# Performance work log

Hardware: AMD Instinct MI355X
Metric: run time of the kernel (lower is better)

Reference implementation:

```python
import jax, jax.numpy as jnp
import numpy as np

# ---------------- geometry constants (from init_kwargs) ----------------
N_PROJ = 96          # cone-beam projections (batch of 2D BP, views of 3D BP)
A2D    = 96          # 2D parallel angles (= detector rows of cone sinogram)
DET2D  = 192         # 2D detector bins   (= detector cols of cone sinogram)
DS2D   = 1.0         # 2D detector spacing
H = 128
W = 128              # intermediate CB_projection image (geom_2d volume)
Zd = 128
Yd = 128
Xd = 128             # reconstruction volume (geometry.volume_shape)
DSO = 500.0          # source-isocenter distance
DSD = 1000.0         # source-detector distance
DU = 3.5
DV = 3.5             # 3D detector spacing (detector grid == H x W image grid)


def _grad_lastdim(x):
    # torch.gradient(x, dim=-1) with unit spacing: central diffs, one-sided edges
    left = x[..., 1:2] - x[..., 0:1]
    mid = (x[..., 2:] - x[..., :-2]) * 0.5
    right = x[..., -1:] - x[..., -2:-1]
    return jnp.concatenate([left, mid, right], axis=-1)


def _image_grid(h, w):
    ys = jnp.arange(h, dtype=jnp.float32) - (h - 1) / 2.0
    xs = jnp.arange(w, dtype=jnp.float32) - (w - 1) / 2.0
    yg, xg = jnp.meshgrid(ys, xs, indexing='ij')  # [h, w]
    return yg, xg


def _weights_3d():
    # Defrise-Clack intermediate-function weighting: cosine of ray angle,
    # w(x,y) = D / sqrt(D^2 + x^2 + y^2) on the intermediate image grid.
    yg, xg = _image_grid(H, W)
    return DSD / jnp.sqrt(DSD * DSD + xg * xg + yg * yg)


def _bp2d(sino):
    # Pixel-driven 2D parallel backprojection, batched over N.
    # sino: [N, A2D, DET2D] -> [N, H, W]
    yg, xg = _image_grid(H, W)
    th = jnp.arange(A2D, dtype=jnp.float32) * (np.pi / A2D)
    s = jnp.cos(th)[:, None, None] * xg + jnp.sin(th)[:, None, None] * yg  # [A,H,W]
    pos = s / DS2D + (DET2D - 1) / 2.0
    i0 = jnp.floor(pos).astype(jnp.int32)
    f = pos - i0
    i1 = i0 + 1
    w0 = jnp.where((i0 >= 0) & (i0 < DET2D), 1.0 - f, 0.0)
    w1 = jnp.where((i1 >= 0) & (i1 < DET2D), f, 0.0)
    i0c = jnp.clip(i0, 0, DET2D - 1)
    i1c = jnp.clip(i1, 0, DET2D - 1)
    aa = jnp.arange(A2D)[:, None, None]  # [A,1,1]
    g0 = sino[:, aa, i0c]  # [N, A, H, W]
    g1 = sino[:, aa, i1c]
    return (g0 * w0 + g1 * w1).sum(axis=1)  # [N, H, W]


def _bp3d(projs):
    # Voxel-driven circular cone-beam backprojection with FDK distance weight.
    # projs: [N_PROJ, H, W] (V=H rows, U=W cols) -> volume [Zd, Yd, Xd]
    zs = jnp.arange(Zd, dtype=jnp.float32) - (Zd - 1) / 2.0
    ys = jnp.arange(Yd, dtype=jnp.float32) - (Yd - 1) / 2.0
    xs = jnp.arange(Xd, dtype=jnp.float32) - (Xd - 1) / 2.0
    zz, yy, xx = jnp.meshgrid(zs, ys, xs, indexing='ij')  # [Z,Y,X]
    betas = jnp.arange(N_PROJ, dtype=jnp.float32) * (2.0 * np.pi / N_PROJ)

    def body(acc, inp):
        beta, proj = inp
        cb, sb = jnp.cos(beta), jnp.sin(beta)
        t = xx * cb + yy * sb          # along central ray
        s = -xx * sb + yy * cb         # transaxial offset
        r = DSO + t                    # source-to-voxel-plane distance
        pu = (DSD * s / r) / DU + (W - 1) / 2.0
        pv = (DSD * zz / r) / DV + (H - 1) / 2.0
        iu0 = jnp.floor(pu).astype(jnp.int32); fu = pu - iu0; iu1 = iu0 + 1
        iv0 = jnp.floor(pv).astype(jnp.int32); fv = pv - iv0; iv1 = iv0 + 1
        mu0 = (iu0 >= 0) & (iu0 < W); mu1 = (iu1 >= 0) & (iu1 < W)
        mv0 = (iv0 >= 0) & (iv0 < H); mv1 = (iv1 >= 0) & (iv1 < H)
        iu0c = jnp.clip(iu0, 0, W - 1); iu1c = jnp.clip(iu1, 0, W - 1)
        iv0c = jnp.clip(iv0, 0, H - 1); iv1c = jnp.clip(iv1, 0, H - 1)
        w00 = jnp.where(mv0 & mu0, (1 - fv) * (1 - fu), 0.0)
        w01 = jnp.where(mv0 & mu1, (1 - fv) * fu, 0.0)
        w10 = jnp.where(mv1 & mu0, fv * (1 - fu), 0.0)
        w11 = jnp.where(mv1 & mu1, fv * fu, 0.0)
        val = (proj[iv0c, iu0c] * w00 + proj[iv0c, iu1c] * w01 +
               proj[iv1c, iu0c] * w10 + proj[iv1c, iu1c] * w11)
        acc = acc + val * (DSD / r) ** 2
        return acc, None

    acc, _ = jax.lax.scan(body, jnp.zeros((Zd, Yd, Xd), jnp.float32), (betas, projs))
    return acc


def setup_inputs() -> dict:
    key = jax.random.key(0)
    k1, k2 = jax.random.split(key)
    sinogram = jax.random.normal(k1, (1, 1, N_PROJ, A2D, DET2D), dtype=jnp.float32)
    weight = jax.random.uniform(k2, (1, N_PROJ, A2D, DET2D), dtype=jnp.float32)
    prelu_weight = jnp.full((1,), 0.25, dtype=jnp.float32)
    return {"sinogram": sinogram, "weight": weight, "prelu_weight": prelu_weight}


def reference(sinogram, weight, prelu_weight):
    ws = sinogram[0] * weight                 # [1, N, A, D]
    deriv = _grad_lastdim(ws)[0]              # [N, A, D]  (squeeze dim 0)
    cb = _bp2d(deriv)                         # [N, H, W]
    weighted_cb = cb * _weights_3d()          # [N, H, W]
    reco = _bp3d(weighted_cb)[None]           # [1, Z, Y, X]
    a = prelu_weight[0]
    return jnp.where(reco >= 0, reco, a * reco)  # PReLU (single parameter)
```

## Files before the change

### kernel.cpp

```cpp
#include <hip/hip_runtime.h>
#include <hip/hip_fp16.h>
#include <math.h>

#define NPROJ 96
#define NANG  96
#define DET   192
#define NPIX  16384
#define SLICE (NANG*DET)

#define WQROW0   16
#define WQROWS   96
#define WQSLICEB (WQROWS*128*16)

#define KPROJ 285.7142857142857f

__device__ __forceinline__ float frcp(float x) { return __builtin_amdgcn_rcpf(x); }

__device__ __forceinline__ float ffract(float x) {
#if __has_builtin(__builtin_amdgcn_fractf)
    return __builtin_amdgcn_fractf(x);
#else
    return x - floorf(x);
#endif
}

typedef __fp16 h2 __attribute__((ext_vector_type(2)));

__device__ __forceinline__ unsigned pack2(float a, float b) {
    h2 p = __builtin_amdgcn_cvt_pkrtz(a, b);
    return __builtin_bit_cast(unsigned, p);
}
__device__ __forceinline__ h2 as_h2(unsigned u) { return __builtin_bit_cast(h2, u); }

#if __has_builtin(__builtin_amdgcn_fdot2)
#define FDOT2(a, b, c) __builtin_amdgcn_fdot2((a), (b), (c), false)
#else
__device__ __forceinline__ float FDOT2(h2 a, h2 b, float c) {
    return c + (float)a[0] * (float)b[0] + (float)a[1] * (float)b[1];
}
#endif

__global__ __launch_bounds__(192) void k_deriv(const float* __restrict__ sino,
                                               const float* __restrict__ wgt,
                                               unsigned* __restrict__ derivp) {
    __shared__ float row[DET];
    const int r = blockIdx.x;
    const int d = threadIdx.x;
    const int base = r * DET + d;
    row[d] = sino[base] * wgt[base];
    __syncthreads();
    auto grad = [&](int i) -> float {
        i = (i > DET-1) ? DET-1 : i;
        if (i == 0)       return row[1] - row[0];
        if (i == DET-1)   return row[DET-1] - row[DET-2];
        return 0.5f * (row[i+1] - row[i-1]);
    };
    const float g0 = grad(d), g1 = grad(d+1);
    derivp[base] = pack2(g0, g1 - g0);
}

__global__ __launch_bounds__(256) void k_bp2d(const unsigned* __restrict__ derivp,
                                              unsigned* __restrict__ wq_dw,
                                              uint2* __restrict__ tbl) {
    __shared__ float sc[NANG], ss[NANG];
    __shared__ float buf[512];
    const int p   = blockIdx.x;
    const int tid = threadIdx.x;

    if (tid < NANG) {
        float s_, c_;
        sincosf((float)tid * (float)(3.14159265358979323846 / 96.0), &s_, &c_);
        sc[tid] = c_; ss[tid] = s_;
    }

    float sb2, cb2;
    sincosf((float)p * (float)(2.0 * 3.14159265358979323846 / 96.0), &sb2, &cb2);

    const int pixbase = blockIdx.y * 512;
    float acc[2], fx[2], fy[2];
    #pragma unroll
    for (int i = 0; i < 2; ++i) {
        const int pix = pixbase + i*256 + tid;
        fx[i] = (float)(pix & 127) - 63.5f;
        fy[i] = (float)(pix >> 7)  - 63.5f;
        acc[i] = 0.0f;
    }
    __syncthreads();

    const unsigned* rowp = derivp + p * SLICE;
    for (int a = 0; a < NANG; ++a, rowp += DET) {
        const float cb = sc[a], sb = ss[a];
        #pragma unroll
        for (int i = 0; i < 2; ++i) {
            const float pos = fmaf(cb, fx[i], fmaf(sb, fy[i], 95.5f));
            const int   i0  = (int)pos;
            const float f   = ffract(pos);
            acc[i] = FDOT2(as_h2(rowp[i0]), as_h2(pack2(1.0f, f)), acc[i]);
        }
    }

    #pragma unroll
    for (int i = 0; i < 2; ++i) {
        const float w = 1000.0f * rsqrtf(1000000.0f + fx[i]*fx[i] + fy[i]*fy[i]);
        buf[i*256 + tid] = acc[i] * w;
    }
    __syncthreads();

    unsigned* sq = wq_dw + p * (WQROWS * 128 * 4);
    uint2*    tp = tbl   + p * NPIX;
    #pragma unroll
    for (int i = 0; i < 2; ++i) {
        const int l   = i*256 + tid;
        const int pix = pixbase + l;
        const int u   = pix & 127;
        const int v   = pix >> 7;
        const float v0 = buf[l];
        const float v1 = (u < 127) ? buf[l + 1] : 0.0f;
        const unsigned pr = pack2(v0, v1 - v0);
        #pragma unroll
        for (int k = 0; k < 4; ++k) {
            const int vb = v - k;
            if (vb >= WQROW0 && vb < WQROW0 + WQROWS)
                sq[(((vb - WQROW0) << 7) + u) << 2 | k] = pr;
        }
        const float t3   = fmaf(fx[i], cb2,  fy[i] * sb2);
        const float sd3  = fmaf(fy[i], cb2, -fx[i] * sb2);
        const float invr = frcp(500.0f + t3);
        const float pu   = fmaf(KPROJ * sd3, invr, 63.5f);
        const int   iu0  = (int)pu;
        const float fu   = ffract(pu);
        float w2 = 1000.0f * invr; w2 *= w2;
        const float Kz   = KPROJ * invr;
        const unsigned kzi = (__builtin_bit_cast(unsigned, Kz) & ~127u) | (unsigned)iu0;
        uint2 e; e.x = pack2(w2, fu * w2); e.y = kzi;
        tp[pix] = e;
    }
}

struct QS {
    uint4    q0, q1;
    unsigned wuw;
    float    fvA0, fvB0, fvA1, fvB1;
    int      d0, d1;
};

__global__ __launch_bounds__(256, 8) void k_bp3d_t2(const unsigned char* __restrict__ wq,
                                                    const unsigned char* __restrict__ tbl8,
                                                    const float* __restrict__ prelu,
                                                    float* __restrict__ out) {
    const int tid = threadIdx.x;
    const int x   = tid & 127;
    const int y   = (blockIdx.x << 1) | (tid >> 7);
    const int z0  = blockIdx.y << 2;
    const int pix = (y << 7) + x;

    const float zlo = (float)z0 - 63.5f;

    float acc[4];
    #pragma unroll
    for (int j = 0; j < 4; ++j) acc[j] = 0.0f;

    const unsigned pixoff = ((unsigned)pix) << 3;

    auto TLOAD = [&](int b) -> uint2 {
        return *(const uint2*)(tbl8 + (pixoff + (unsigned)b * (NPIX * 8u)));
    };

    auto ISSUE = [&](QS& S, uint2 T, int b) {
        S.wuw = T.x;
        const int   iu0 = (int)(T.y & 127u);
        const float Kz  = __builtin_bit_cast(float, T.y & ~127u);
        const unsigned sbase = (unsigned)b * (unsigned)WQSLICEB
                             + (unsigned)(iu0 << 4) - (unsigned)(WQROW0 << 11);

        const float pvA0 = fmaf(Kz, zlo, 63.5f);
        const float pvB0 = pvA0 + Kz;
        const int   ivA0 = (int)pvA0;
        S.d0   = (int)pvB0 - ivA0;
        S.fvA0 = ffract(pvA0);
        S.fvB0 = ffract(pvB0);
        S.q0   = *(const uint4*)(wq + (sbase + ((unsigned)ivA0 << 11)));

        const float pvA1 = fmaf(Kz, zlo + 2.0f, 63.5f);
        const float pvB1 = pvA1 + Kz;
        const int   ivA1 = (int)pvA1;
        S.d1   = (int)pvB1 - ivA1;
        S.fvA1 = ffract(pvA1);
        S.fvB1 = ffract(pvB1);
        S.q1   = *(const uint4*)(wq + (sbase + ((unsigned)ivA1 << 11)));
    };

    auto MATH = [&](const QS& S) {
        const h2 wuw = as_h2(S.wuw);
        {
            const float tA = FDOT2(as_h2(S.q0.x), wuw, 0.0f);
            const float bA = FDOT2(as_h2(S.q0.y), wuw, 0.0f);
            acc[0] += fmaf(S.fvA0, bA - tA, tA);
            const unsigned tBv = S.d0 ? S.q0.y : S.q0.x;
            const unsigned bBv = S.d0 ? S.q0.z : S.q0.y;
            const float tB = FDOT2(as_h2(tBv), wuw, 0.0f);
            const float bB = FDOT2(as_h2(bBv), wuw, 0.0f);
            acc[1] += fmaf(S.fvB0, bB - tB, tB);
        }
        {
            const float tA = FDOT2(as_h2(S.q1.x), wuw, 0.0f);
            const float bA = FDOT2(as_h2(S.q1.y), wuw, 0.0f);
            acc[2] += fmaf(S.fvA1, bA - tA, tA);
            const unsigned tBv = S.d1 ? S.q1.y : S.q1.x;
            const unsigned bBv = S.d1 ? S.q1.z : S.q1.y;
            const float tB = FDOT2(as_h2(tBv), wuw, 0.0f);
            const float bB = FDOT2(as_h2(bBv), wuw, 0.0f);
            acc[3] += fmaf(S.fvB1, bB - tB, tB);
        }
    };

    QS qa, qb;
    uint2 Ta = TLOAD(0);
    uint2 Tb = TLOAD(1);
    ISSUE(qa, Ta, 0);
    for (int b = 0; b < 94; b += 2) {
        Ta = TLOAD(b + 2);
        ISSUE(qb, Tb, b + 1);
        MATH(qa);
        Tb = TLOAD(b + 3);
        ISSUE(qa, Ta, b + 2);
        MATH(qb);
    }
    ISSUE(qb, Tb, 95);
    MATH(qa);
    MATH(qb);

    const float a = prelu[0];
    #pragma unroll
    for (int j = 0; j < 4; ++j) {
        const float v = acc[j];
        out[((z0 + j) << 14) + (y << 7) + x] = (v >= 0.0f) ? v : a * v;
    }
}

extern "C" void kernel_launch(void* const* d_in, const int* in_sizes, int n_in,
                              void* d_out, int out_size, void* d_ws, size_t ws_size,
                              hipStream_t stream) {
    const float* sino  = (const float*)d_in[0];
    const float* wgt   = (const float*)d_in[1];
    const float* prelu = (const float*)d_in[2];
    float* out = (float*)d_out;

    unsigned char* wsb = (unsigned char*)d_ws;
    unsigned* wq_dw  = (unsigned*)wsb;
    uint2*    tbl    = (uint2*)(wsb + (size_t)NPROJ * WQSLICEB);
    unsigned* derivp = (unsigned*)(wsb + (size_t)NPROJ * WQSLICEB
                                       + (size_t)NPROJ * NPIX * 8);

    k_deriv  <<<dim3(NPROJ * NANG), dim3(192), 0, stream>>>(sino, wgt, derivp);
    k_bp2d   <<<dim3(NPROJ, 32),    dim3(256), 0, stream>>>(derivp, wq_dw, tbl);
    k_bp3d_t2<<<dim3(64, 32),       dim3(256), 0, stream>>>((const unsigned char*)wq_dw,
                                                            (const unsigned char*)tbl, prelu, out);
}
```

Measured before the change: 180.5 us.

## Batch derivative rows per block and share 2D BP geometry across four projections

The derivative kernel now processes 16 sinogram rows per 256-thread block instead of one 192-thread block per row, which cuts launch granularity. The 2D backprojection kernel gives each thread one pixel across four projections. The per-angle position, index and fraction are computed once and reused for four gathers, so address arithmetic is amortised and there are more independent loads in flight. The trade-off is fewer pixels per thread, higher register use and a different grid shape for the bp2d stage. The 3D backprojection, which likely dominates the runtime, is unchanged.

```diff
diff --git a/kernel.cpp b/kernel.cpp
--- a/kernel.cpp
+++ b/kernel.cpp
@@ -7,6 +7,7 @@
 #define DET   192
 #define NPIX  16384
 #define SLICE (NANG*DET)
+#define NROWS (NPROJ*NANG)
 
 #define WQROW0   16
 #define WQROWS   96
@@ -40,91 +41,111 @@
 }
 #endif
 
-__global__ __launch_bounds__(192) void k_deriv(const float* __restrict__ sino,
-                                               const float* __restrict__ wgt,
-                                               unsigned* __restrict__ derivp) {
-    __shared__ float row[DET];
-    const int r = blockIdx.x;
-    const int d = threadIdx.x;
-    const int base = r * DET + d;
-    row[d] = sino[base] * wgt[base];
+__global__ __launch_bounds__(256) void k_deriv16(const float* __restrict__ sino,
+                                                 const float* __restrict__ wgt,
+                                                 unsigned* __restrict__ derivp) {
+    __shared__ float sw[16 * DET];
+    const int tid   = threadIdx.x;
+    const int base0 = blockIdx.x * (16 * DET);
+
+    #pragma unroll
+    for (int k = 0; k < 12; ++k) {
+        const int i = k * 256 + tid;
+        sw[i] = sino[base0 + i] * wgt[base0 + i];
+    }
     __syncthreads();
-    auto grad = [&](int i) -> float {
-        i = (i > DET-1) ? DET-1 : i;
-        if (i == 0)       return row[1] - row[0];
-        if (i == DET-1)   return row[DET-1] - row[DET-2];
-        return 0.5f * (row[i+1] - row[i-1]);
-    };
-    const float g0 = grad(d), g1 = grad(d+1);
-    derivp[base] = pack2(g0, g1 - g0);
-}
-
-__global__ __launch_bounds__(256) void k_bp2d(const unsigned* __restrict__ derivp,
-                                              unsigned* __restrict__ wq_dw,
-                                              uint2* __restrict__ tbl) {
+
+    #pragma unroll
+    for (int k = 0; k < 12; ++k) {
+        const int i = k * 256 + tid;
+        const int r = i / DET;
+        const int d = i - r * DET;
+        const float* row = sw + r * DET;
+        auto grad = [&](int q) -> float {
+            if (q == 0)        return row[1] - row[0];
+            if (q >= DET - 1)  return row[DET-1] - row[DET-2];
+            return 0.5f * (row[q+1] - row[q-1]);
+        };
+        const float g0 = grad(d), g1 = grad(d + 1);
+        derivp[base0 + i] = pack2(g0, g1 - g0);
+    }
+}
+
+__global__ __launch_bounds__(256) void k_bp2d_p4(const unsigned* __restrict__ derivp,
+                                                 unsigned* __restrict__ wq_dw,
+                                                 uint2* __restrict__ tbl) {
     __shared__ float sc[NANG], ss[NANG];
-    __shared__ float buf[512];
-    const int p   = blockIdx.x;
+    __shared__ float sc3[4], ss3[4];
+    __shared__ float buf[4][257];
     const int tid = threadIdx.x;
+    const int p0  = blockIdx.y << 2;
+    const int pix = (blockIdx.x << 8) + tid;
+    const int u   = pix & 127;
+    const int v   = pix >> 7;
 
     if (tid < NANG) {
         float s_, c_;
         sincosf((float)tid * (float)(3.14159265358979323846 / 96.0), &s_, &c_);
         sc[tid] = c_; ss[tid] = s_;
     }
-
-    float sb2, cb2;
-    sincosf((float)p * (float)(2.0 * 3.14159265358979323846 / 96.0), &sb2, &cb2);
-
-    const int pixbase = blockIdx.y * 512;
-    float acc[2], fx[2], fy[2];
-    #pragma unroll
-    for (int i = 0; i < 2; ++i) {
-        const int pix = pixbase + i*256 + tid;
-        fx[i] = (float)(pix & 127) - 63.5f;
-        fy[i] = (float)(pix >> 7)  - 63.5f;
-        acc[i] = 0.0f;
-    }
+    if (tid < 4) {
+        float s_, c_;
+        sincosf((float)(p0 + tid) * (float)(2.0 * 3.14159265358979323846 / 96.0), &s_, &c_);
+        sc3[tid] = c_; ss3[tid] = s_;
+    }
+
+    const float fx = (float)u - 63.5f;
+    const float fy = (float)v - 63.5f;
+
+    float acc[4];
+    #pragma unroll
+    for (int j = 0; j < 4; ++j) acc[j] = 0.0f;
+
     __syncthreads();
 
-    const unsigned* rowp = derivp + p * SLICE;
-    for (int a = 0; a < NANG; ++a, rowp += DET) {
+    const unsigned* b0 = derivp + (p0 + 0) * SLICE;
+    const unsigned* b1 = derivp + (p0 + 1) * SLICE;
+    const unsigned* b2 = derivp + (p0 + 2) * SLICE;
+    const unsigned* b3 = derivp + (p0 + 3) * SLICE;
+
+    int aoff = 0;
+    #pragma unroll 2
+    for (int a = 0; a < NANG; ++a, aoff += DET) {
         const float cb = sc[a], sb = ss[a];
-        #pragma unroll
-        for (int i = 0; i < 2; ++i) {
-            const float pos = fmaf(cb, fx[i], fmaf(sb, fy[i], 95.5f));
-            const int   i0  = (int)pos;
-            const float f   = ffract(pos);
-            acc[i] = FDOT2(as_h2(rowp[i0]), as_h2(pack2(1.0f, f)), acc[i]);
-        }
-    }
-
-    #pragma unroll
-    for (int i = 0; i < 2; ++i) {
-        const float w = 1000.0f * rsqrtf(1000000.0f + fx[i]*fx[i] + fy[i]*fy[i]);
-        buf[i*256 + tid] = acc[i] * w;
+        const float pos = fmaf(cb, fx, fmaf(sb, fy, 95.5f));
+        const int   i0  = (int)pos;
+        const float f   = ffract(pos);
+        const h2    wv  = as_h2(pack2(1.0f, f));
+        const int   idx = aoff + i0;
+        acc[0] = FDOT2(as_h2(b0[idx]), wv, acc[0]);
+        acc[1] = FDOT2(as_h2(b1[idx]), wv, acc[1]);
+        acc[2] = FDOT2(as_h2(b2[idx]), wv, acc[2]);
+        acc[3] = FDOT2(as_h2(b3[idx]), wv, acc[3]);
+    }
+
+    const float w = 1000.0f * rsqrtf(1000000.0f + fx*fx + fy*fy);
+    #pragma unroll
+    for (int j = 0; j < 4; ++j) {
+        acc[j] *= w;
+        buf[j][tid] = acc[j];
     }
     __syncthreads();
 
-    unsigned* sq = wq_dw + p * (WQROWS * 128 * 4);
-    uint2*    tp = tbl   + p * NPIX;
-    #pragma unroll
-    for (int i = 0; i < 2; ++i) {
-        const int l   = i*256 + tid;
-        const int pix = pixbase + l;
-        const int u   = pix & 127;
-        const int v   = pix >> 7;
-        const float v0 = buf[l];
-        const float v1 = (u < 127) ? buf[l + 1] : 0.0f;
+    #pragma unroll
+    for (int j = 0; j < 4; ++j) {
+        const float v0 = acc[j];
+        const float v1 = (u < 127) ? buf[j][tid + 1] : 0.0f;
         const unsigned pr = pack2(v0, v1 - v0);
+        unsigned* sq = wq_dw + (p0 + j) * (WQROWS * 128 * 4);
         #pragma unroll
         for (int k = 0; k < 4; ++k) {
             const int vb = v - k;
             if (vb >= WQROW0 && vb < WQROW0 + WQROWS)
                 sq[(((vb - WQROW0) << 7) + u) << 2 | k] = pr;
         }
-        const float t3   = fmaf(fx[i], cb2,  fy[i] * sb2);
-        const float sd3  = fmaf(fy[i], cb2, -fx[i] * sb2);
+        const float cb3  = sc3[j], sb3 = ss3[j];
+        const float t3   = fmaf(fx, cb3,  fy * sb3);
+        const float sd3  = fmaf(fy, cb3, -fx * sb3);
         const float invr = frcp(500.0f + t3);
         const float pu   = fmaf(KPROJ * sd3, invr, 63.5f);
         const int   iu0  = (int)pu;
@@ -133,7 +154,7 @@
         const float Kz   = KPROJ * invr;
         const unsigned kzi = (__builtin_bit_cast(unsigned, Kz) & ~127u) | (unsigned)iu0;
         uint2 e; e.x = pack2(w2, fu * w2); e.y = kzi;
-        tp[pix] = e;
+        tbl[(p0 + j) * NPIX + pix] = e;
     }
 }
 
@@ -252,8 +273,8 @@
     unsigned* derivp = (unsigned*)(wsb + (size_t)NPROJ * WQSLICEB
                                        + (size_t)NPROJ * NPIX * 8);
 
-    k_deriv  <<<dim3(NPROJ * NANG), dim3(192), 0, stream>>>(sino, wgt, derivp);
-    k_bp2d   <<<dim3(NPROJ, 32),    dim3(256), 0, stream>>>(derivp, wq_dw, tbl);
-    k_bp3d_t2<<<dim3(64, 32),       dim3(256), 0, stream>>>((const unsigned char*)wq_dw,
-                                                            (const unsigned char*)tbl, prelu, out);
-}
+    k_deriv16<<<dim3(NROWS / 16),  dim3(256), 0, stream>>>(sino, wgt, derivp);
+    k_bp2d_p4<<<dim3(64, 24),      dim3(256), 0, stream>>>(derivp, wq_dw, tbl);
+    k_bp3d_t2<<<dim3(64, 32),      dim3(256), 0, stream>>>((const unsigned char*)wq_dw,
+                                                           (const unsigned char*)tbl, prelu, out);
+}
```

Result: no change. 180.8 us (+0.2%).
